# Optimization experiments

Measured on AMD Instinct MI355X. Metric: run time of the kernel, lower is better.

## Reference

```python
import jax, jax.numpy as jnp
import numpy as np

HEADS = 8
DK = 64   # key_size (defaults to size_per_head)
DV = 64   # size_per_head
RATE = 4
OUT = HEADS * DV  # 512


def extract_seq_patches(x, kernel, rate):
    # x: [b, L, d] -> [b, L, kernel, d]; strided local window gather
    b, L, d = x.shape
    k_size = kernel + (rate - 1) * (kernel - 1)
    p_right = (k_size - 1) // 2
    p_left = k_size - 1 - p_right
    xp = jnp.pad(x, ((0, 0), (p_left, p_right), (0, 0)))
    patches = [xp[:, i:i + L] for i in range(0, k_size, rate)]  # kernel slices
    return jnp.stack(patches, axis=2)


def setup_inputs() -> dict:
    key = jax.random.key(0)
    k1, k2, k3, k4 = jax.random.split(key, 4)
    s = 1.0 / np.sqrt(OUT)
    x = jax.random.normal(k1, (2, 4096, OUT), dtype=jnp.float32)
    Wq = jax.random.normal(k2, (OUT, HEADS * DK), dtype=jnp.float32) * s
    Wk = jax.random.normal(k3, (OUT, HEADS * DK), dtype=jnp.float32) * s
    Wv = jax.random.normal(k4, (OUT, HEADS * DV), dtype=jnp.float32) * s
    return {"x": x, "Wq": Wq, "Wk": Wk, "Wv": Wv}


def reference(x, Wq, Wk, Wv):
    b, L, d = x.shape
    pad = RATE - L % RATE  # torch code always pads (pad=RATE when L % RATE == 0)
    xpad = jnp.pad(x, ((0, 0), (0, pad), (0, 0)))
    nL = L + pad
    n = nL // RATE
    kernel = 2 * RATE - 1  # 1 + 2*neighbors

    qw = xpad @ Wq
    kw = xpad @ Wk
    vw = xpad @ Wv

    kwp = extract_seq_patches(kw, kernel, RATE)  # [b, nL, K, H*dk]
    vwp = extract_seq_patches(vw, kernel, RATE)  # [b, nL, K, H*dv]

    # [b, h, r, n, d]
    qw = qw.reshape(b, n, RATE, HEADS, DK).transpose(0, 3, 2, 1, 4)
    kw = kw.reshape(b, n, RATE, HEADS, DK).transpose(0, 3, 2, 1, 4)
    vw = vw.reshape(b, n, RATE, HEADS, DV).transpose(0, 3, 2, 1, 4)
    # [b, h, r, n, K, d]
    kwp = kwp.reshape(b, n, RATE, kernel, HEADS, DK).transpose(0, 4, 2, 1, 3, 5)
    vwp = vwp.reshape(b, n, RATE, kernel, HEADS, DV).transpose(0, 4, 2, 1, 3, 5)

    scale = 1.0 / np.sqrt(DK)
    a = jnp.einsum('bhrnd,bhrmd->bhrnm', qw, kw) * scale    # strided scores [b,h,r,n,n]
    ap = jnp.einsum('bhrnd,bhrnkd->bhrnk', qw, kwp) * scale  # local scores  [b,h,r,n,K]

    A = jax.nn.softmax(jnp.concatenate([a, ap], axis=-1), axis=-1)
    a, ap = A[..., :n], A[..., n:]

    o = jnp.einsum('bhrnm,bhrmd->bhrnd', a, vw) + jnp.einsum('bhrnk,bhrnkd->bhrnd', ap, vwp)
    o = o.transpose(0, 3, 2, 1, 4).reshape(b, nL, HEADS * DV)
    return o[:, :L]
```

## Files before the change

### kernel.cpp

```cpp
#include <hip/hip_runtime.h>
#include <hip/hip_bf16.h>


#define BATCH 2
#define LSEQ  4096
#define DMODEL 512
#define NH    8
#define DHEAD 64
#define NPAD  1088
#define QSCALE 0.18033688011112042f

typedef __bf16 bf16x8 __attribute__((ext_vector_type(8)));
typedef __attribute__((ext_vector_type(4))) float f32x4;
typedef unsigned short u16;
typedef unsigned int u32;
typedef __attribute__((ext_vector_type(8))) u16 u16x8;
typedef __attribute__((ext_vector_type(4))) u16 u16x4;

__device__ __forceinline__ u16 f2bf(float f) {
    u32 u = __float_as_uint(f);
    u += 0x7fffu + ((u >> 16) & 1u);
    return (u16)(u >> 16);
}

__device__ __forceinline__ u16 cvt_bf(float f) {
    __bf16 t = (__bf16)f;
    return *(const u16*)&t;
}

__device__ __forceinline__ void gload16(const u16* g, u16* l) {
    __builtin_amdgcn_global_load_lds(
        (const __attribute__((address_space(1))) u32*)(const void*)g,
        (__attribute__((address_space(3))) u32*)(void*)l, 16, 0, 0);
}

__global__ __launch_bounds__(256) void prep_kernel(
    const float* __restrict__ x,
    const float* __restrict__ Wq, const float* __restrict__ Wk, const float* __restrict__ Wv,
    u16* __restrict__ xb, u16* __restrict__ Wt)
{
    const int bid = blockIdx.x, tid = threadIdx.x;
    if (bid < 2048) {
        const size_t i0 = (size_t)bid * 2048 + (size_t)tid * 8;
        float4 a = *(const float4*)(x + i0);
        float4 b = *(const float4*)(x + i0 + 4);
        u16x8 o = { f2bf(a.x), f2bf(a.y), f2bf(a.z), f2bf(a.w),
                    f2bf(b.x), f2bf(b.y), f2bf(b.z), f2bf(b.w) };
        *(u16x8*)(xb + i0) = o;
    } else {
        const int wb  = bid - 2048;
        const int mat = wb >> 6;
        const int t   = wb & 63;
        const int k0  = (t >> 3) * 64, c0 = (t & 7) * 64;
        const float* W = (mat == 0) ? Wq : (mat == 1) ? Wk : Wv;
        __shared__ u16 Ws[64][72];
        #pragma unroll
        for (int i = 0; i < 4; ++i) {
            const int chunk = i * 256 + tid;
            const int kr = chunk >> 4, c4 = (chunk & 15) * 4;
            float4 v = *(const float4*)(W + (size_t)(k0 + kr) * DMODEL + c0 + c4);
            u16x4 q = { f2bf(v.x), f2bf(v.y), f2bf(v.z), f2bf(v.w) };
            *(u16x4*)&Ws[kr][c4] = q;
        }
        __syncthreads();
        const int cc = tid >> 2, kq = (tid & 3) * 16;
        alignas(16) u16 tmp[16];
        #pragma unroll
        for (int kk = 0; kk < 16; ++kk) tmp[kk] = Ws[kq + kk][cc];
        u16* dst = Wt + (size_t)(mat * 512 + c0 + cc) * DMODEL + k0 + kq;
        *(u16x8*)dst       = *(const u16x8*)&tmp[0];
        *(u16x8*)(dst + 8) = *(const u16x8*)&tmp[8];
    }
}

__global__ __launch_bounds__(256) void gemm_kernel(
    const u16* __restrict__ xb, const u16* __restrict__ Wt,
    u16* __restrict__ Qb, u16* __restrict__ Kb, u16* __restrict__ Vb)
{
    const int bid = blockIdx.x;
    const int xcd = bid & 7;
    const int j   = bid >> 3;
    const int mt  = xcd * 8 + (j / 12);
    const int nt  = j % 12;
    const int m0 = mt * 128;
    const int n0 = nt * 128;
    const int tid = threadIdx.x;
    const int w = tid >> 6, l = tid & 63, lr = l & 15, lh = l >> 4;
    const int wr = w >> 1, wc = w & 1;

    __shared__ u16 smem[16896];
    u16* As = smem;
    u16* Bs = smem + 8192;

    f32x4 acc[4][4];
    const f32x4 fzero = {0.f, 0.f, 0.f, 0.f};
    #pragma unroll
    for (int mi = 0; mi < 4; ++mi)
        #pragma unroll
        for (int nj = 0; nj < 4; ++nj) acc[mi][nj] = fzero;

    for (int kt = 0; kt < 8; ++kt) {
        const int k0 = kt * 64;
        #pragma unroll
        for (int i = 0; i < 4; ++i) {
            const int cid = i * 256 + tid;
            const int row = cid >> 3, ch = cid & 7;
            const int sch = ch ^ (row & 7);
            u16* dstA = As + (i * 256 + w * 64) * 8;
            u16* dstB = Bs + (i * 256 + w * 64) * 8;
            gload16(xb + (size_t)(m0 + row) * DMODEL + k0 + sch * 8, dstA);
            gload16(Wt + (size_t)(n0 + row) * DMODEL + k0 + sch * 8, dstB);
        }
        __syncthreads();

        #pragma unroll
        for (int kk = 0; kk < 2; ++kk) {
            const int cs = (kk * 4 + lh) ^ (lr & 7);
            bf16x8 af[4], bfr[4];
            #pragma unroll
            for (int mi = 0; mi < 4; ++mi)
                af[mi] = *(const bf16x8*)(As + (wr * 64 + mi * 16 + lr) * 64 + cs * 8);
            #pragma unroll
            for (int nj = 0; nj < 4; ++nj)
                bfr[nj] = *(const bf16x8*)(Bs + (wc * 64 + nj * 16 + lr) * 64 + cs * 8);
            #pragma unroll
            for (int mi = 0; mi < 4; ++mi)
                #pragma unroll
                for (int nj = 0; nj < 4; ++nj)
                    acc[mi][nj] = __builtin_amdgcn_mfma_f32_16x16x32_bf16(af[mi], bfr[nj], acc[mi][nj], 0, 0, 0);
        }
        __syncthreads();
    }

    const int mat = nt >> 2;
    const int hp  = nt & 3;
    if (mat < 2) {
        u16* Ob = (mat == 0) ? Qb : Kb;
        const float osc = (mat == 0) ? QSCALE : 1.0f;
        #pragma unroll
        for (int mi = 0; mi < 4; ++mi) {
            const int gmb = m0 + wr * 64 + mi * 16 + lh * 4;
            const int b = gmb >> 12;
            #pragma unroll
            for (int rr = 0; rr < 4; ++rr) {
                const int t = (gmb + rr) & 4095;
                const int n = t >> 2, r = t & 3;
                #pragma unroll
                for (int nj = 0; nj < 4; ++nj) {
                    const int c  = wc * 64 + nj * 16 + lr;
                    const int h  = hp * 2 + (c >> 6);
                    const int dk = c & 63;
                    const size_t g = ((size_t)(b * NH + h)) * 4 + r;
                    Ob[(g * NPAD + n) * DHEAD + dk] = f2bf(acc[mi][nj][rr] * osc);
                }
            }
        }
    } else {
        #pragma unroll
        for (int mi = 0; mi < 4; ++mi) {
            const int nrel = wr * 16 + mi * 4 + lh;
            #pragma unroll
            for (int nj = 0; nj < 4; ++nj) {
                const int c = wc * 64 + nj * 16 + lr;
                #pragma unroll
                for (int rr = 0; rr < 4; ++rr)
                    smem[c * 132 + rr * 32 + nrel] = f2bf(acc[mi][nj][rr]);
            }
        }
        __syncthreads();
        const int b  = m0 >> 12;
        const int nb = (m0 & 4095) >> 2;
        #pragma unroll
        for (int e = 0; e < 2; ++e) {
            const int chunk = e * 256 + tid;
            const int c = chunk & 127, r = chunk >> 7;
            const int h  = hp * 2 + (c >> 6);
            const int dv = c & 63;
            const size_t g = ((size_t)(b * NH + h)) * 4 + r;
            u16* dst = Vb + (g * DHEAD + dv) * NPAD + nb;
            const u16* src = smem + c * 132 + r * 32;
            alignas(16) u16 tmp[32];
            #pragma unroll
            for (int q8 = 0; q8 < 8; ++q8)
                *(u16x4*)&tmp[q8 * 4] = *(const u16x4*)(src + q8 * 4);
            #pragma unroll
            for (int q16 = 0; q16 < 4; ++q16)
                *(u16x8*)(dst + q16 * 8) = *(const u16x8*)&tmp[q16 * 8];
        }
    }
}

__global__ __launch_bounds__(512) void attn_kernel(
    const u16* __restrict__ Qb, const u16* __restrict__ Kb, const u16* __restrict__ Vb,
    float* __restrict__ out)
{
    const int g  = blockIdx.x;
    const int b  = g >> 5;
    const int h  = (g >> 2) & 7;
    const int r  = g & 3;
    const int q0 = blockIdx.y * 128;
    const int tid = threadIdx.x;
    const int w  = tid >> 6;
    const int l  = tid & 63;
    const int lr = l & 15, lh = l >> 4;

    const u16* Qg  = Qb + (size_t)g * NPAD * DHEAD;
    const u16* Kg  = Kb + (size_t)g * NPAD * DHEAD;
    const u16* Vtg = Vb + (size_t)g * DHEAD * NPAD;

    __shared__ u16 KV[3][2][4096];
    __shared__ u16 Ps[8][16][68];

    const int srow = tid >> 3;
    const int ssch = (tid & 7) ^ (srow & 7);
    const u16* ksrc0 = Kg  + (size_t)srow * DHEAD + ssch * 8;
    const u16* vsrc0 = Vtg + (size_t)srow * NPAD  + ssch * 8;

    bf16x8 qa[2];
    {
        const u16* qrow = Qg + (size_t)(q0 + w * 16 + lr) * DHEAD;
        qa[0] = *(const bf16x8*)(qrow + lh * 8);
        qa[1] = *(const bf16x8*)(qrow + 32 + lh * 8);
    }

    const f32x4 fzero = {0.f, 0.f, 0.f, 0.f};
    f32x4 o[4];
    #pragma unroll
    for (int j = 0; j < 4; ++j) o[j] = fzero;
    float Lpart[4] = {0.f, 0.f, 0.f, 0.f};

    const int qw0 = q0 + w * 16;

    gload16(ksrc0,              &KV[0][0][w * 512]);
    gload16(vsrc0,              &KV[0][1][w * 512]);
    gload16(ksrc0 + 64 * DHEAD, &KV[1][0][w * 512]);
    gload16(vsrc0 + 64,         &KV[1][1][w * 512]);

    for (int mt = 0; mt < 16; ++mt) {
        if (mt < 15) asm volatile("s_waitcnt vmcnt(2)" ::: "memory");
        else         asm volatile("s_waitcnt vmcnt(0)" ::: "memory");
        __builtin_amdgcn_s_barrier();
        if (mt < 14) {
            const int nb = (mt + 2) % 3;
            gload16(ksrc0 + (size_t)(mt + 2) * 64 * DHEAD, &KV[nb][0][w * 512]);
            gload16(vsrc0 + (mt + 2) * 64,                 &KV[nb][1][w * 512]);
        }

        const u16* Kbuf = KV[mt % 3][0];
        const u16* Vbuf = KV[mt % 3][1];

        f32x4 s[4];
        __builtin_amdgcn_s_setprio(1);
        #pragma unroll
        for (int ni = 0; ni < 4; ++ni) {
            const int rbase = (ni * 16 + lr) * 8;
            const int sl0 = lh ^ (lr & 7), sl1 = (4 + lh) ^ (lr & 7);
            bf16x8 kb0 = *(const bf16x8*)(Kbuf + (rbase + sl0) * 8);
            bf16x8 kb1 = *(const bf16x8*)(Kbuf + (rbase + sl1) * 8);
            f32x4 t = __builtin_amdgcn_mfma_f32_16x16x32_bf16(qa[0], kb0, fzero, 0, 0, 0);
            s[ni] = __builtin_amdgcn_mfma_f32_16x16x32_bf16(qa[1], kb1, t, 0, 0, 0);
        }
        __builtin_amdgcn_s_setprio(0);

        const int m0 = mt * 64;
        const bool special = (m0 + 66 >= qw0) && (m0 <= qw0 + 18);
        if (!special) {
            #pragma unroll
            for (int ni = 0; ni < 4; ++ni) {
                #pragma unroll
                for (int rr = 0; rr < 4; ++rr) {
                    const float p = __builtin_amdgcn_exp2f(s[ni][rr]);
                    Lpart[rr] += p;
                    Ps[w][lh * 4 + rr][ni * 16 + lr] = cvt_bf(p);
                }
            }
        } else {
            #pragma unroll
            for (int ni = 0; ni < 4; ++ni) {
                const int mg = m0 + ni * 16 + lr;
                #pragma unroll
                for (int rr = 0; rr < 4; ++rr) {
                    const int qg = qw0 + lh * 4 + rr;
                    float v = s[ni][rr];
                    const int dd = mg - qg;
                    if (dd >= -3 && dd <= 3) v += 1.0f;
                    const float p = __builtin_amdgcn_exp2f(v);
                    Lpart[rr] += p;
                    Ps[w][lh * 4 + rr][ni * 16 + lr] = cvt_bf(p);
                }
            }
        }

        __builtin_amdgcn_s_setprio(1);
        #pragma unroll
        for (int kk = 0; kk < 2; ++kk) {
            const int slot = (kk * 4 + lh) ^ (lr & 7);
            bf16x8 pa = *(const bf16x8*)&Ps[w][lr][kk * 32 + lh * 8];
            #pragma unroll
            for (int j = 0; j < 4; ++j) {
                bf16x8 vb = *(const bf16x8*)(Vbuf + ((j * 16 + lr) * 8 + slot) * 8);
                o[j] = __builtin_amdgcn_mfma_f32_16x16x32_bf16(pa, vb, o[j], 0, 0, 0);
            }
        }
        __builtin_amdgcn_s_setprio(0);
    }

    #pragma unroll
    for (int rr = 0; rr < 4; ++rr) {
        float s_ = Lpart[rr];
        #pragma unroll
        for (int off = 1; off < 16; off <<= 1)
            s_ += __shfl_xor(s_, off, 16);
        const int qg = qw0 + lh * 4 + rr;
        const int coob = (qg < 3 ? 3 - qg : 0) + (qg > 1021 ? qg - 1021 : 0);
        const float extra = (float)(coob + 1 + (qg >= 1021 ? 1 : 0));
        const float inv = 1.0f / (s_ + extra);
        const int t = qg * 4 + r;
        float* orow = out + ((size_t)b * LSEQ + t) * DMODEL + h * DHEAD;
        #pragma unroll
        for (int j = 0; j < 4; ++j)
            orow[j * 16 + lr] = o[j][rr] * inv;
    }
}

extern "C" void kernel_launch(void* const* d_in, const int* in_sizes, int n_in,
                              void* d_out, int out_size, void* d_ws, size_t ws_size,
                              hipStream_t stream) {
    const float* x  = (const float*)d_in[0];
    const float* Wq = (const float*)d_in[1];
    const float* Wk = (const float*)d_in[2];
    const float* Wv = (const float*)d_in[3];
    float* out = (float*)d_out;

    const size_t SZ = (size_t)BATCH * NH * 4 * NPAD * DHEAD;
    u16* Qb = (u16*)d_ws;
    u16* Kb = Qb + SZ;
    u16* Vb = Kb + SZ;

    u16* xb = (u16*)d_out;
    u16* Wt = xb + (size_t)8192 * 512;

    prep_kernel<<<2240, 256, 0, stream>>>(x, Wq, Wk, Wv, xb, Wt);

    gemm_kernel<<<768, 256, 0, stream>>>(xb, Wt, Qb, Kb, Vb);

    dim3 ga(64, 8);
    attn_kernel<<<ga, 512, 0, stream>>>(Qb, Kb, Vb, out);
}
```

Baseline: 65.41 us.

## Software-pipeline QK^T scores one tile ahead of softmax and PV

```diff
diff --git a/kernel.cpp b/kernel.cpp
--- a/kernel.cpp
+++ b/kernel.cpp
@@ -190,7 +190,7 @@
     }
 }
 
-__global__ __launch_bounds__(512) void attn_kernel(
+__global__ __launch_bounds__(512, 4) void attn_kernel(
     const u16* __restrict__ Qb, const u16* __restrict__ Kb, const u16* __restrict__ Vb,
     float* __restrict__ out)
 {
@@ -230,15 +230,32 @@
     float Lpart[4] = {0.f, 0.f, 0.f, 0.f};
 
     const int qw0 = q0 + w * 16;
+    const int sl0 = lh ^ (lr & 7), sl1 = (4 + lh) ^ (lr & 7);
 
     gload16(ksrc0,              &KV[0][0][w * 512]);
     gload16(vsrc0,              &KV[0][1][w * 512]);
     gload16(ksrc0 + 64 * DHEAD, &KV[1][0][w * 512]);
     gload16(vsrc0 + 64,         &KV[1][1][w * 512]);
+    asm volatile("s_waitcnt vmcnt(2)" ::: "memory");
+    __builtin_amdgcn_s_barrier();
+
+    f32x4 sn[4];
+    {
+        const u16* Kbuf = KV[0][0];
+        __builtin_amdgcn_s_setprio(1);
+        #pragma unroll
+        for (int ni = 0; ni < 4; ++ni) {
+            const int rbase = (ni * 16 + lr) * 8;
+            bf16x8 kb0 = *(const bf16x8*)(Kbuf + (rbase + sl0) * 8);
+            bf16x8 kb1 = *(const bf16x8*)(Kbuf + (rbase + sl1) * 8);
+            f32x4 t = __builtin_amdgcn_mfma_f32_16x16x32_bf16(qa[0], kb0, fzero, 0, 0, 0);
+            sn[ni] = __builtin_amdgcn_mfma_f32_16x16x32_bf16(qa[1], kb1, t, 0, 0, 0);
+        }
+        __builtin_amdgcn_s_setprio(0);
+    }
 
     for (int mt = 0; mt < 16; ++mt) {
-        if (mt < 15) asm volatile("s_waitcnt vmcnt(2)" ::: "memory");
-        else         asm volatile("s_waitcnt vmcnt(0)" ::: "memory");
+        asm volatile("s_waitcnt vmcnt(0)" ::: "memory");
         __builtin_amdgcn_s_barrier();
         if (mt < 14) {
             const int nb = (mt + 2) % 3;
@@ -246,21 +263,18 @@
             gload16(vsrc0 + (mt + 2) * 64,                 &KV[nb][1][w * 512]);
         }
 
-        const u16* Kbuf = KV[mt % 3][0];
         const u16* Vbuf = KV[mt % 3][1];
-
-        f32x4 s[4];
-        __builtin_amdgcn_s_setprio(1);
-        #pragma unroll
-        for (int ni = 0; ni < 4; ++ni) {
-            const int rbase = (ni * 16 + lr) * 8;
-            const int sl0 = lh ^ (lr & 7), sl1 = (4 + lh) ^ (lr & 7);
-            bf16x8 kb0 = *(const bf16x8*)(Kbuf + (rbase + sl0) * 8);
-            bf16x8 kb1 = *(const bf16x8*)(Kbuf + (rbase + sl1) * 8);
-            f32x4 t = __builtin_amdgcn_mfma_f32_16x16x32_bf16(qa[0], kb0, fzero, 0, 0, 0);
-            s[ni] = __builtin_amdgcn_mfma_f32_16x16x32_bf16(qa[1], kb1, t, 0, 0, 0);
-        }
-        __builtin_amdgcn_s_setprio(0);
+        const u16* Kn   = KV[(mt + 1) % 3][0];
+
+        bf16x8 kb0[4], kb1[4];
+        if (mt < 15) {
+            #pragma unroll
+            for (int ni = 0; ni < 4; ++ni) {
+                const int rbase = (ni * 16 + lr) * 8;
+                kb0[ni] = *(const bf16x8*)(Kn + (rbase + sl0) * 8);
+                kb1[ni] = *(const bf16x8*)(Kn + (rbase + sl1) * 8);
+            }
+        }
 
         const int m0 = mt * 64;
         const bool special = (m0 + 66 >= qw0) && (m0 <= qw0 + 18);
@@ -269,7 +283,7 @@
             for (int ni = 0; ni < 4; ++ni) {
                 #pragma unroll
                 for (int rr = 0; rr < 4; ++rr) {
-                    const float p = __builtin_amdgcn_exp2f(s[ni][rr]);
+                    const float p = __builtin_amdgcn_exp2f(sn[ni][rr]);
                     Lpart[rr] += p;
                     Ps[w][lh * 4 + rr][ni * 16 + lr] = cvt_bf(p);
                 }
@@ -281,7 +295,7 @@
                 #pragma unroll
                 for (int rr = 0; rr < 4; ++rr) {
                     const int qg = qw0 + lh * 4 + rr;
-                    float v = s[ni][rr];
+                    float v = sn[ni][rr];
                     const int dd = mg - qg;
                     if (dd >= -3 && dd <= 3) v += 1.0f;
                     const float p = __builtin_amdgcn_exp2f(v);
@@ -289,6 +303,16 @@
                     Ps[w][lh * 4 + rr][ni * 16 + lr] = cvt_bf(p);
                 }
             }
+        }
+
+        if (mt < 15) {
+            __builtin_amdgcn_s_setprio(1);
+            #pragma unroll
+            for (int ni = 0; ni < 4; ++ni) {
+                f32x4 t = __builtin_amdgcn_mfma_f32_16x16x32_bf16(qa[0], kb0[ni], fzero, 0, 0, 0);
+                sn[ni] = __builtin_amdgcn_mfma_f32_16x16x32_bf16(qa[1], kb1[ni], t, 0, 0, 0);
+            }
+            __builtin_amdgcn_s_setprio(0);
         }
 
         __builtin_amdgcn_s_setprio(1);
```

After: 66.01 us. No clear change (+0.9%).

## Fuse x fp32-to-bf16 conversion into GEMM A-tile load

Applied to the files above, without the earlier changes.

```diff
diff --git a/kernel.cpp b/kernel.cpp
--- a/kernel.cpp
+++ b/kernel.cpp
@@ -16,6 +16,7 @@
 typedef unsigned int u32;
 typedef __attribute__((ext_vector_type(8))) u16 u16x8;
 typedef __attribute__((ext_vector_type(4))) u16 u16x4;
+typedef __attribute__((ext_vector_type(4))) u32 u32x4;
 
 __device__ __forceinline__ u16 f2bf(float f) {
     u32 u = __float_as_uint(f);
@@ -28,53 +29,49 @@
     return *(const u16*)&t;
 }
 
-__device__ __forceinline__ void gload16(const u16* g, u16* l) {
+__device__ __forceinline__ u32 cvtpk(float lo, float hi) {
+    u32 d;
+    asm("v_cvt_pk_bf16_f32 %0, %1, %2" : "=v"(d) : "v"(lo), "v"(hi));
+    return d;
+}
+
+__device__ __forceinline__ void gload16(const void* g, void* l) {
     __builtin_amdgcn_global_load_lds(
-        (const __attribute__((address_space(1))) u32*)(const void*)g,
-        (__attribute__((address_space(3))) u32*)(void*)l, 16, 0, 0);
+        (const __attribute__((address_space(1))) u32*)g,
+        (__attribute__((address_space(3))) u32*)l, 16, 0, 0);
 }
 
 __global__ __launch_bounds__(256) void prep_kernel(
-    const float* __restrict__ x,
     const float* __restrict__ Wq, const float* __restrict__ Wk, const float* __restrict__ Wv,
-    u16* __restrict__ xb, u16* __restrict__ Wt)
+    u16* __restrict__ Wt)
 {
-    const int bid = blockIdx.x, tid = threadIdx.x;
-    if (bid < 2048) {
-        const size_t i0 = (size_t)bid * 2048 + (size_t)tid * 8;
-        float4 a = *(const float4*)(x + i0);
-        float4 b = *(const float4*)(x + i0 + 4);
-        u16x8 o = { f2bf(a.x), f2bf(a.y), f2bf(a.z), f2bf(a.w),
-                    f2bf(b.x), f2bf(b.y), f2bf(b.z), f2bf(b.w) };
-        *(u16x8*)(xb + i0) = o;
-    } else {
-        const int wb  = bid - 2048;
-        const int mat = wb >> 6;
-        const int t   = wb & 63;
-        const int k0  = (t >> 3) * 64, c0 = (t & 7) * 64;
-        const float* W = (mat == 0) ? Wq : (mat == 1) ? Wk : Wv;
-        __shared__ u16 Ws[64][72];
-        #pragma unroll
-        for (int i = 0; i < 4; ++i) {
-            const int chunk = i * 256 + tid;
-            const int kr = chunk >> 4, c4 = (chunk & 15) * 4;
-            float4 v = *(const float4*)(W + (size_t)(k0 + kr) * DMODEL + c0 + c4);
-            u16x4 q = { f2bf(v.x), f2bf(v.y), f2bf(v.z), f2bf(v.w) };
-            *(u16x4*)&Ws[kr][c4] = q;
-        }
-        __syncthreads();
-        const int cc = tid >> 2, kq = (tid & 3) * 16;
-        alignas(16) u16 tmp[16];
-        #pragma unroll
-        for (int kk = 0; kk < 16; ++kk) tmp[kk] = Ws[kq + kk][cc];
-        u16* dst = Wt + (size_t)(mat * 512 + c0 + cc) * DMODEL + k0 + kq;
-        *(u16x8*)dst       = *(const u16x8*)&tmp[0];
-        *(u16x8*)(dst + 8) = *(const u16x8*)&tmp[8];
-    }
+    const int wb  = blockIdx.x;
+    const int tid = threadIdx.x;
+    const int mat = wb >> 6;
+    const int t   = wb & 63;
+    const int k0  = (t >> 3) * 64, c0 = (t & 7) * 64;
+    const float* W = (mat == 0) ? Wq : (mat == 1) ? Wk : Wv;
+    __shared__ u16 Ws[64][72];
+    #pragma unroll
+    for (int i = 0; i < 4; ++i) {
+        const int chunk = i * 256 + tid;
+        const int kr = chunk >> 4, c4 = (chunk & 15) * 4;
+        float4 v = *(const float4*)(W + (size_t)(k0 + kr) * DMODEL + c0 + c4);
+        u16x4 q = { f2bf(v.x), f2bf(v.y), f2bf(v.z), f2bf(v.w) };
+        *(u16x4*)&Ws[kr][c4] = q;
+    }
+    __syncthreads();
+    const int cc = tid >> 2, kq = (tid & 3) * 16;
+    alignas(16) u16 tmp[16];
+    #pragma unroll
+    for (int kk = 0; kk < 16; ++kk) tmp[kk] = Ws[kq + kk][cc];
+    u16* dst = Wt + (size_t)(mat * 512 + c0 + cc) * DMODEL + k0 + kq;
+    *(u16x8*)dst       = *(const u16x8*)&tmp[0];
+    *(u16x8*)(dst + 8) = *(const u16x8*)&tmp[8];
 }
 
 __global__ __launch_bounds__(256) void gemm_kernel(
-    const u16* __restrict__ xb, const u16* __restrict__ Wt,
+    const float* __restrict__ x, const u16* __restrict__ Wt,
     u16* __restrict__ Qb, u16* __restrict__ Kb, u16* __restrict__ Vb)
 {
     const int bid = blockIdx.x;
@@ -88,9 +85,10 @@
     const int w = tid >> 6, l = tid & 63, lr = l & 15, lh = l >> 4;
     const int wr = w >> 1, wc = w & 1;
 
-    __shared__ u16 smem[16896];
-    u16* As = smem;
-    u16* Bs = smem + 8192;
+    __shared__ __align__(16) u32 smem32[12288];
+    float* As32 = (float*)smem32;
+    u16*   Bs   = (u16*)(smem32 + 8192);
+    u16*   Vr   = (u16*)smem32;
 
     f32x4 acc[4][4];
     const f32x4 fzero = {0.f, 0.f, 0.f, 0.f};
@@ -106,10 +104,16 @@
             const int cid = i * 256 + tid;
             const int row = cid >> 3, ch = cid & 7;
             const int sch = ch ^ (row & 7);
-            u16* dstA = As + (i * 256 + w * 64) * 8;
-            u16* dstB = Bs + (i * 256 + w * 64) * 8;
-            gload16(xb + (size_t)(m0 + row) * DMODEL + k0 + sch * 8, dstA);
-            gload16(Wt + (size_t)(n0 + row) * DMODEL + k0 + sch * 8, dstB);
+            gload16(Wt + (size_t)(n0 + row) * DMODEL + k0 + sch * 8,
+                    Bs + (i * 256 + w * 64) * 8);
+        }
+        #pragma unroll
+        for (int i = 0; i < 8; ++i) {
+            const int cid = i * 256 + tid;
+            const int row = cid >> 4, hc = cid & 15;
+            const int shc = hc ^ ((row & 7) << 1);
+            gload16(x + (size_t)(m0 + row) * DMODEL + k0 + shc * 4,
+                    As32 + (size_t)(i * 256 + w * 64) * 4);
         }
         __syncthreads();
 
@@ -118,8 +122,14 @@
             const int cs = (kk * 4 + lh) ^ (lr & 7);
             bf16x8 af[4], bfr[4];
             #pragma unroll
-            for (int mi = 0; mi < 4; ++mi)
-                af[mi] = *(const bf16x8*)(As + (wr * 64 + mi * 16 + lr) * 64 + cs * 8);
+            for (int mi = 0; mi < 4; ++mi) {
+                const float* ap = As32 + ((size_t)(wr * 64 + mi * 16 + lr) * 64 + cs * 8);
+                float4 a0 = *(const float4*)ap;
+                float4 a1 = *(const float4*)(ap + 4);
+                u32x4 av = { cvtpk(a0.x, a0.y), cvtpk(a0.z, a0.w),
+                             cvtpk(a1.x, a1.y), cvtpk(a1.z, a1.w) };
+                af[mi] = __builtin_bit_cast(bf16x8, av);
+            }
             #pragma unroll
             for (int nj = 0; nj < 4; ++nj)
                 bfr[nj] = *(const bf16x8*)(Bs + (wc * 64 + nj * 16 + lr) * 64 + cs * 8);
@@ -164,7 +174,7 @@
                 const int c = wc * 64 + nj * 16 + lr;
                 #pragma unroll
                 for (int rr = 0; rr < 4; ++rr)
-                    smem[c * 132 + rr * 32 + nrel] = f2bf(acc[mi][nj][rr]);
+                    Vr[c * 132 + rr * 32 + nrel] = f2bf(acc[mi][nj][rr]);
             }
         }
         __syncthreads();
@@ -178,7 +188,7 @@
             const int dv = c & 63;
             const size_t g = ((size_t)(b * NH + h)) * 4 + r;
             u16* dst = Vb + (g * DHEAD + dv) * NPAD + nb;
-            const u16* src = smem + c * 132 + r * 32;
+            const u16* src = Vr + c * 132 + r * 32;
             alignas(16) u16 tmp[32];
             #pragma unroll
             for (int q8 = 0; q8 < 8; ++q8)
@@ -337,12 +347,11 @@
     u16* Kb = Qb + SZ;
     u16* Vb = Kb + SZ;
 
-    u16* xb = (u16*)d_out;
-    u16* Wt = xb + (size_t)8192 * 512;
-
-    prep_kernel<<<2240, 256, 0, stream>>>(x, Wq, Wk, Wv, xb, Wt);
-
-    gemm_kernel<<<768, 256, 0, stream>>>(xb, Wt, Qb, Kb, Vb);
+    u16* Wt = (u16*)d_out;
+
+    prep_kernel<<<192, 256, 0, stream>>>(Wq, Wk, Wv, Wt);
+
+    gemm_kernel<<<768, 256, 0, stream>>>(x, Wt, Qb, Kb, Vb);
 
     dim3 ga(64, 8);
     attn_kernel<<<ga, 512, 0, stream>>>(Qb, Kb, Vb, out);
```

After: 68.85 us. +5.3%, slower.
